# Kernel optimization log

Measured on AMD Instinct MI355X. Metric: run time of the kernel, lower is better.

Reference implementation:

```python
import jax, jax.numpy as jnp
import numpy as np

DIM = 1024
HEADS = 16
DIM_HEAD = 64
INNER = HEADS * DIM_HEAD  # 1024
SCALE = 1.0 / DIM_HEAD ** 0.5


def setup_inputs() -> dict:
    key = jax.random.key(0)
    ks = jax.random.split(key, 5)
    x = jax.random.normal(ks[0], (4, 2048, DIM), dtype=jnp.float32)
    # nn.Linear weights stored as [out, in]; we keep [in, out] for x @ W
    Wq = jax.random.normal(ks[1], (DIM, INNER), dtype=jnp.float32) * (1.0 / np.sqrt(DIM))
    Wkv = jax.random.normal(ks[2], (DIM, 2 * INNER), dtype=jnp.float32) * (1.0 / np.sqrt(DIM))
    Wo = jax.random.normal(ks[3], (INNER, DIM), dtype=jnp.float32) * (1.0 / np.sqrt(INNER))
    bo = jax.random.normal(ks[4], (DIM,), dtype=jnp.float32) * 0.01
    return {"x": x, "Wq": Wq, "Wkv": Wkv, "Wo": Wo, "bo": bo}


def reference(x, Wq, Wkv, Wo, bo):
    b, n, _ = x.shape
    q = x @ Wq                      # [b, n, inner]
    kv = x @ Wkv                    # [b, n, 2*inner]
    k, v = jnp.split(kv, 2, axis=2)
    # 'b n (h d) -> b h n d'
    q = q.reshape(b, n, HEADS, DIM_HEAD).transpose(0, 2, 1, 3)
    k = k.reshape(b, n, HEADS, DIM_HEAD).transpose(0, 2, 1, 3)
    v = v.reshape(b, n, HEADS, DIM_HEAD).transpose(0, 2, 1, 3)
    scores = jnp.einsum('bhid,bhjd->bhij', q, k) * SCALE  # [b,h,n,n]
    attn = jax.nn.softmax(scores, axis=-1)
    out = jnp.einsum('bhij,bhjd->bhid', attn, v)          # [b,h,n,d]
    out = out.transpose(0, 2, 1, 3).reshape(b, n, INNER)  # 'b h n d -> b n (h d)'
    return out @ Wo + bo
```

## Files before the change

kernel.cpp:

```cpp
#include <hip/hip_runtime.h>
#include <hip/hip_bf16.h>

typedef unsigned short u16;
typedef unsigned int u32;
typedef __attribute__((ext_vector_type(8))) short s8v;
typedef __attribute__((ext_vector_type(4))) float f4v;
typedef __attribute__((ext_vector_type(4))) unsigned short u16x4;

#define MFMA16(a,b,c) __builtin_amdgcn_mfma_f32_16x16x32_bf16((a),(b),(c),0,0,0)

#define TOKENS 8192
#define SEQ    2048
#define NH     16
#define DH     64
#define DIMK   1024
#define QPRE   0.18033688f

#if defined(__has_builtin)
#if __has_builtin(__builtin_amdgcn_exp2f)
#define EXP2(x) __builtin_amdgcn_exp2f(x)
#else
#define EXP2(x) __expf((x) * 0.69314718f)
#endif
#else
#define EXP2(x) __expf((x) * 0.69314718f)
#endif

__device__ __forceinline__ u16 f2bf(float x){
  union { float f; u32 u; } v; v.f = x;
  u32 r = v.u + 0x7FFFu + ((v.u >> 16) & 1u);
  return (u16)(r >> 16);
}

__device__ __forceinline__ void gld16(const u16* g, u16* s){
  __builtin_amdgcn_global_load_lds(
      (const __attribute__((address_space(1))) unsigned int*)(const void*)g,
      (__attribute__((address_space(3))) unsigned int*)(void*)s,
      16, 0, 0);
}

__global__ __launch_bounds__(256) void k_cast(const float* __restrict__ src,
                                              u16* __restrict__ dst){
  int i = (blockIdx.x * 256 + threadIdx.x) * 4;
  float4 v = *(const float4*)(src + i);
  u16x4 vh;
  float a[4] = {v.x, v.y, v.z, v.w};
#pragma unroll
  for (int j = 0; j < 4; j++) vh[j] = f2bf(a[j]);
  *(u16x4*)(dst + i) = vh;
}

__global__ __launch_bounds__(256) void k_transpose(const float* __restrict__ s0, int c0,
                                                   const float* __restrict__ s1, int c1,
                                                   int K, u16* __restrict__ dh){
  __shared__ float tile[64][65];
  int nb = blockIdx.x * 64, kb = blockIdx.y * 64;
  int tr = threadIdx.x >> 6, tc = threadIdx.x & 63;
#pragma unroll
  for (int i = 0; i < 16; i++){
    int k = kb + tr + i * 4, n = nb + tc;
    float v = (n < c0) ? s0[(size_t)k * c0 + n] : s1[(size_t)k * c1 + (n - c0)];
    tile[tr + i * 4][tc] = v;
  }
  __syncthreads();
#pragma unroll
  for (int i = 0; i < 16; i++){
    int nl = tr + i * 4, kl = tc;
    dh[(size_t)(nb + nl) * K + (kb + kl)] = f2bf(tile[kl][nl]);
  }
}

__global__ __launch_bounds__(256) void k_gemm(
    const u16* __restrict__ A, const u16* __restrict__ B, int nx,
    int mode, const float* __restrict__ bias, float* __restrict__ Cf,
    u16* __restrict__ Qh, u16* __restrict__ Kh, u16* __restrict__ Vth)
{
  __shared__ u16 sA[2][128*32], sB[2][128*32];
  const int tid = threadIdx.x, wave = tid >> 6, lane = tid & 63;
  const int lm = lane & 15, quad = lane >> 4;

  const int bid = blockIdx.x;
  const int xcd = bid & 7, slot = bid >> 3;
  const int gpx = nx >> 3;
  const int xt = xcd * gpx + slot % gpx;
  const int yt = slot / gpx;
  const int m0 = yt * 128, n0 = xt * 128;

  const int cof = (lane & 3) * 8;
  const int rsub = lane >> 2;

  f4v acc[4][4];
#pragma unroll
  for (int i = 0; i < 4; i++)
#pragma unroll
    for (int j = 0; j < 4; j++) acc[i][j] = (f4v){0.f, 0.f, 0.f, 0.f};

  const int wm = (wave >> 1) * 64, wn = (wave & 1) * 64;

  for (int kc = 0; kc < 16; kc++){
    int k = kc * 64;
#pragma unroll
    for (int cc = 0; cc < 2; cc++)
#pragma unroll
      for (int half = 0; half < 2; half++){
        int rb = wave * 32 + half * 16;
        int r = rb + rsub;
        gld16(A + (size_t)(m0 + r) * DIMK + k + cc * 32 + cof, &sA[cc][rb * 32]);
        gld16(B + (size_t)(n0 + r) * DIMK + k + cc * 32 + cof, &sB[cc][rb * 32]);
      }
    __syncthreads();

#pragma unroll
    for (int cc = 0; cc < 2; cc++){
      s8v ah[4], bh[4];
#pragma unroll
      for (int i = 0; i < 4; i++){
        ah[i] = *(const s8v*)&sA[cc][(wm + i * 16 + lm) * 32 + quad * 8];
        bh[i] = *(const s8v*)&sB[cc][(wn + i * 16 + lm) * 32 + quad * 8];
      }
#pragma unroll
      for (int i = 0; i < 4; i++)
#pragma unroll
        for (int j = 0; j < 4; j++)
          acc[i][j] = MFMA16(ah[i], bh[j], acc[i][j]);
    }
    __syncthreads();
  }

  if (mode == 1){
#pragma unroll
    for (int i = 0; i < 4; i++)
#pragma unroll
      for (int j = 0; j < 4; j++){
        int gn = n0 + wn + j * 16 + lm;
        float bv = bias[gn];
#pragma unroll
        for (int r = 0; r < 4; r++){
          int gm = m0 + wm + i * 16 + quad * 4 + r;
          Cf[(size_t)gm * DIMK + gn] = acc[i][j][r] + bv;
        }
      }
  } else {
#pragma unroll
    for (int i = 0; i < 4; i++)
#pragma unroll
      for (int j = 0; j < 4; j++){
        int gn = n0 + wn + j * 16 + lm;
#pragma unroll
        for (int r = 0; r < 4; r++){
          int gm = m0 + wm + i * 16 + quad * 4 + r;
          float v = acc[i][j][r];
          if (gn < 1024){
            Qh[(size_t)gm * DIMK + gn] = f2bf(v * QPRE);
          } else if (gn < 2048){
            Kh[(size_t)gm * DIMK + (gn - 1024)] = f2bf(v);
          } else {
            int df = gn - 2048;
            int hh = df >> 6, dd = df & 63;
            int bb = gm >> 11, ii = gm & 2047;
            int ip = (ii & ~31) | (((ii & 15) << 1) | ((ii >> 4) & 1));
            Vth[(size_t)((bb * NH + hh) * DH + dd) * SEQ + ip] = f2bf(v);
          }
        }
      }
  }
}

__global__ __launch_bounds__(256, 4) void k_attn(
    const u16* __restrict__ Qh, const u16* __restrict__ Kh, const u16* __restrict__ Vth,
    u16* __restrict__ Oh)
{
  __shared__ u16 sK[2*64*32];
  __shared__ u16 sV[2*64*32];
  __shared__ u16 sP[2*128*32];
  u32* sPd = (u32*)sP;

  const int bid = blockIdx.x;
  const int xcd = bid & 7, slot = bid >> 3;
  const int g = xcd * 8 + (slot >> 4);
  const int qt = slot & 15;
  const int b = g >> 4, h = g & 15;

  const int tid = threadIdx.x, wave = tid >> 6, lane = tid & 63;
  const int lm = lane & 15, quad = lane >> 4;
  const int tok0 = b * SEQ + qt * 128;
  const int cof = (lane & 3) * 8;
  const int rsub = lane >> 2;

  s8v qf[2][2];
#pragma unroll
  for (int c = 0; c < 2; c++)
#pragma unroll
    for (int ifr = 0; ifr < 2; ifr++){
      size_t ga = (size_t)(tok0 + wave * 32 + ifr * 16 + lm) * DIMK + h * DH + c * 32 + quad * 8;
      qf[c][ifr] = *(const s8v*)(Qh + ga);
    }

  const f4v fz = (f4v){0.f, 0.f, 0.f, 0.f};

  float lpart[2][4];
  f4v oacc[2][4];
#pragma unroll
  for (int ifr = 0; ifr < 2; ifr++){
#pragma unroll
    for (int r = 0; r < 4; r++) lpart[ifr][r] = 0.f;
#pragma unroll
    for (int fd = 0; fd < 4; fd++) oacc[ifr][fd] = (f4v){0.f, 0.f, 0.f, 0.f};
  }

  for (int kt = 0; kt < 32; kt++){
    int j0 = kt * 64;
#pragma unroll
    for (int c = 0; c < 2; c++){
      size_t gk = (size_t)(b * SEQ + j0 + wave * 16 + rsub) * DIMK + h * DH + c * 32 + cof;
      gld16(Kh + gk, &sK[c * 2048 + wave * 512]);
      size_t gv = (size_t)((b * NH + h) * DH + wave * 16 + rsub) * SEQ + j0 + c * 32 + cof;
      gld16(Vth + gv, &sV[c * 2048 + wave * 512]);
    }
    __syncthreads();

    f4v s[2][4];
#pragma unroll
    for (int fn = 0; fn < 4; fn++){
      s8v kh0 = *(const s8v*)&sK[0 * 2048 + (fn * 16 + lm) * 32 + quad * 8];
      s8v kh1 = *(const s8v*)&sK[1 * 2048 + (fn * 16 + lm) * 32 + quad * 8];
#pragma unroll
      for (int ifr = 0; ifr < 2; ifr++){
        s[ifr][fn] = MFMA16(qf[0][ifr], kh0, fz);
        s[ifr][fn] = MFMA16(qf[1][ifr], kh1, s[ifr][fn]);
      }
    }

#pragma unroll
    for (int ifr = 0; ifr < 2; ifr++){
#pragma unroll
      for (int fn = 0; fn < 4; fn++)
#pragma unroll
        for (int r = 0; r < 4; r++)
          s[ifr][fn][r] = EXP2(s[ifr][fn][r]);
      int rowb = wave * 32 + ifr * 16 + quad * 4;
#pragma unroll
      for (int r = 0; r < 4; r++)
#pragma unroll
        for (int jc = 0; jc < 2; jc++){
          union { float f; u32 u; } a0, a1;
          a0.f = s[ifr][jc * 2 + 0][r];
          a1.f = s[ifr][jc * 2 + 1][r];
          lpart[ifr][r] += a0.f + a1.f;
          sPd[jc * 2048 + (rowb + r) * 16 + lm] = __builtin_amdgcn_perm(a1.u, a0.u, 0x07060302);
        }
    }

#pragma unroll
    for (int c = 0; c < 2; c++)
#pragma unroll
      for (int ifr = 0; ifr < 2; ifr++){
        s8v ph = *(const s8v*)&sP[c * 4096 + (wave * 32 + ifr * 16 + lm) * 32 + quad * 8];
#pragma unroll
        for (int fd = 0; fd < 4; fd++){
          s8v vh = *(const s8v*)&sV[c * 2048 + (fd * 16 + lm) * 32 + quad * 8];
          oacc[ifr][fd] = MFMA16(ph, vh, oacc[ifr][fd]);
        }
      }
    __syncthreads();
  }

#pragma unroll
  for (int ifr = 0; ifr < 2; ifr++){
#pragma unroll
    for (int off = 1; off < 16; off <<= 1)
#pragma unroll
      for (int r = 0; r < 4; r++)
        lpart[ifr][r] += __shfl_xor(lpart[ifr][r], off, 64);
    float inv[4];
#pragma unroll
    for (int r = 0; r < 4; r++) inv[r] = 1.f / lpart[ifr][r];
#pragma unroll
    for (int fd = 0; fd < 4; fd++){
      int dcol = h * DH + fd * 16 + lm;
#pragma unroll
      for (int r = 0; r < 4; r++){
        int tok = tok0 + wave * 32 + ifr * 16 + quad * 4 + r;
        Oh[(size_t)tok * DIMK + dcol] = f2bf(oacc[ifr][fd][r] * inv[r]);
      }
    }
  }
}

extern "C" void kernel_launch(void* const* d_in, const int* in_sizes, int n_in,
                              void* d_out, int out_size, void* d_ws, size_t ws_size,
                              hipStream_t stream) {
  const float* x   = (const float*)d_in[0];
  const float* Wq  = (const float*)d_in[1];
  const float* Wkv = (const float*)d_in[2];
  const float* Wo  = (const float*)d_in[3];
  const float* bo  = (const float*)d_in[4];
  float* out = (float*)d_out;

  char* ws = (char*)d_ws;
  size_t off = 0;
  auto alloc = [&](size_t bytes) -> u16* {
    u16* p = (u16*)(ws + off);
    off += (bytes + 255) & ~(size_t)255;
    return p;
  };
  const size_t TK2 = (size_t)TOKENS * DIMK * 2;
  u16* xh  = alloc(TK2);
  u16* Wh  = alloc((size_t)3072 * DIMK * 2);
  u16* WOh = alloc((size_t)1024 * DIMK * 2);
  u16* Qh  = alloc(TK2);
  u16* Kh  = alloc(TK2);
  u16* Vth = alloc(TK2);
  u16* Oh  = alloc(TK2);

  k_cast<<<dim3((TOKENS * DIMK) / 1024), 256, 0, stream>>>(x, xh);
  k_transpose<<<dim3(48, 16), 256, 0, stream>>>(Wq, 1024, Wkv, 2048, DIMK, Wh);
  k_transpose<<<dim3(16, 16), 256, 0, stream>>>(Wo, 1024, Wo, 1024, DIMK, WOh);
  k_gemm<<<dim3(24 * 64), 256, 0, stream>>>(xh, Wh, 24, 0, nullptr, nullptr, Qh, Kh, Vth);
  k_attn<<<dim3(16 * NH * 4), 256, 0, stream>>>(Qh, Kh, Vth, Oh);
  k_gemm<<<dim3(8 * 64), 256, 0, stream>>>(Oh, WOh, 8, 1, bo, out, nullptr, nullptr, nullptr);
}
```

Baseline: 309.2 us.

## Double-buffer GEMM A tiles and attention K/V tiles, load B from global

```diff
diff --git a/kernel.cpp b/kernel.cpp
--- a/kernel.cpp
+++ b/kernel.cpp
@@ -71,19 +71,26 @@
 }
 
 __global__ __launch_bounds__(256) void k_gemm(
-    const u16* __restrict__ A, const u16* __restrict__ B, int nx,
+    const u16* __restrict__ A, const u16* __restrict__ B, int nx, int mpart,
     int mode, const float* __restrict__ bias, float* __restrict__ Cf,
     u16* __restrict__ Qh, u16* __restrict__ Kh, u16* __restrict__ Vth)
 {
-  __shared__ u16 sA[2][128*32], sB[2][128*32];
+  __shared__ u16 sA[2][2][128*32];
   const int tid = threadIdx.x, wave = tid >> 6, lane = tid & 63;
   const int lm = lane & 15, quad = lane >> 4;
 
   const int bid = blockIdx.x;
   const int xcd = bid & 7, slot = bid >> 3;
-  const int gpx = nx >> 3;
-  const int xt = xcd * gpx + slot % gpx;
-  const int yt = slot / gpx;
+  int xt, yt;
+  if (mpart == 0){
+    const int gpx = nx >> 3;
+    xt = xcd * gpx + slot % gpx;
+    yt = slot / gpx;
+  } else {
+    const int mg = (int)(gridDim.x >> 3) / nx;
+    xt = slot % nx;
+    yt = xcd * mg + slot / nx;
+  }
   const int m0 = yt * 128, n0 = xt * 128;
 
   const int cof = (lane & 3) * 8;
@@ -97,32 +104,44 @@
 
   const int wm = (wave >> 1) * 64, wn = (wave & 1) * 64;
 
-  for (int kc = 0; kc < 16; kc++){
+  auto stageA = [&](int kc, int db){
     int k = kc * 64;
 #pragma unroll
     for (int cc = 0; cc < 2; cc++)
 #pragma unroll
       for (int half = 0; half < 2; half++){
         int rb = wave * 32 + half * 16;
-        int r = rb + rsub;
-        gld16(A + (size_t)(m0 + r) * DIMK + k + cc * 32 + cof, &sA[cc][rb * 32]);
-        gld16(B + (size_t)(n0 + r) * DIMK + k + cc * 32 + cof, &sB[cc][rb * 32]);
-      }
-    __syncthreads();
+        gld16(A + (size_t)(m0 + rb + rsub) * DIMK + k + cc * 32 + cof,
+              &sA[db][cc][rb * 32]);
+      }
+  };
+
+  stageA(0, 0);
+  __syncthreads();
+
+  for (int kc = 0; kc < 16; kc++){
+    const int db = kc & 1;
+    if (kc + 1 < 16) stageA(kc + 1, db ^ 1);
+
+    s8v bfr[2][4];
+#pragma unroll
+    for (int cc = 0; cc < 2; cc++)
+#pragma unroll
+      for (int j = 0; j < 4; j++)
+        bfr[cc][j] = *(const s8v*)(B + (size_t)(n0 + wn + j * 16 + lm) * DIMK
+                                     + kc * 64 + cc * 32 + quad * 8);
 
 #pragma unroll
     for (int cc = 0; cc < 2; cc++){
-      s8v ah[4], bh[4];
-#pragma unroll
-      for (int i = 0; i < 4; i++){
-        ah[i] = *(const s8v*)&sA[cc][(wm + i * 16 + lm) * 32 + quad * 8];
-        bh[i] = *(const s8v*)&sB[cc][(wn + i * 16 + lm) * 32 + quad * 8];
-      }
+      s8v ah[4];
 #pragma unroll
       for (int i = 0; i < 4; i++)
+        ah[i] = *(const s8v*)&sA[db][cc][(wm + i * 16 + lm) * 32 + quad * 8];
+#pragma unroll
+      for (int i = 0; i < 4; i++)
 #pragma unroll
         for (int j = 0; j < 4; j++)
-          acc[i][j] = MFMA16(ah[i], bh[j], acc[i][j]);
+          acc[i][j] = MFMA16(ah[i], bfr[cc][j], acc[i][j]);
     }
     __syncthreads();
   }
@@ -166,12 +185,12 @@
   }
 }
 
-__global__ __launch_bounds__(256, 4) void k_attn(
+__global__ __launch_bounds__(256, 3) void k_attn(
     const u16* __restrict__ Qh, const u16* __restrict__ Kh, const u16* __restrict__ Vth,
     u16* __restrict__ Oh)
 {
-  __shared__ u16 sK[2*64*32];
-  __shared__ u16 sV[2*64*32];
+  __shared__ u16 sK[2][2*64*32];
+  __shared__ u16 sV[2][2*64*32];
   __shared__ u16 sP[2*128*32];
   u32* sPd = (u32*)sP;
 
@@ -208,22 +227,29 @@
     for (int fd = 0; fd < 4; fd++) oacc[ifr][fd] = (f4v){0.f, 0.f, 0.f, 0.f};
   }
 
-  for (int kt = 0; kt < 32; kt++){
+  auto stageKV = [&](int kt, int db){
     int j0 = kt * 64;
 #pragma unroll
     for (int c = 0; c < 2; c++){
       size_t gk = (size_t)(b * SEQ + j0 + wave * 16 + rsub) * DIMK + h * DH + c * 32 + cof;
-      gld16(Kh + gk, &sK[c * 2048 + wave * 512]);
+      gld16(Kh + gk, &sK[db][c * 2048 + wave * 512]);
       size_t gv = (size_t)((b * NH + h) * DH + wave * 16 + rsub) * SEQ + j0 + c * 32 + cof;
-      gld16(Vth + gv, &sV[c * 2048 + wave * 512]);
-    }
-    __syncthreads();
+      gld16(Vth + gv, &sV[db][c * 2048 + wave * 512]);
+    }
+  };
+
+  stageKV(0, 0);
+  __syncthreads();
+
+  for (int kt = 0; kt < 32; kt++){
+    const int db = kt & 1;
+    if (kt + 1 < 32) stageKV(kt + 1, db ^ 1);
 
     f4v s[2][4];
 #pragma unroll
     for (int fn = 0; fn < 4; fn++){
-      s8v kh0 = *(const s8v*)&sK[0 * 2048 + (fn * 16 + lm) * 32 + quad * 8];
-      s8v kh1 = *(const s8v*)&sK[1 * 2048 + (fn * 16 + lm) * 32 + quad * 8];
+      s8v kh0 = *(const s8v*)&sK[db][0 * 2048 + (fn * 16 + lm) * 32 + quad * 8];
+      s8v kh1 = *(const s8v*)&sK[db][1 * 2048 + (fn * 16 + lm) * 32 + quad * 8];
 #pragma unroll
       for (int ifr = 0; ifr < 2; ifr++){
         s[ifr][fn] = MFMA16(qf[0][ifr], kh0, fz);
@@ -258,7 +284,7 @@
         s8v ph = *(const s8v*)&sP[c * 4096 + (wave * 32 + ifr * 16 + lm) * 32 + quad * 8];
 #pragma unroll
         for (int fd = 0; fd < 4; fd++){
-          s8v vh = *(const s8v*)&sV[c * 2048 + (fd * 16 + lm) * 32 + quad * 8];
+          s8v vh = *(const s8v*)&sV[db][c * 2048 + (fd * 16 + lm) * 32 + quad * 8];
           oacc[ifr][fd] = MFMA16(ph, vh, oacc[ifr][fd]);
         }
       }
@@ -316,7 +342,9 @@
   k_cast<<<dim3((TOKENS * DIMK) / 1024), 256, 0, stream>>>(x, xh);
   k_transpose<<<dim3(48, 16), 256, 0, stream>>>(Wq, 1024, Wkv, 2048, DIMK, Wh);
   k_transpose<<<dim3(16, 16), 256, 0, stream>>>(Wo, 1024, Wo, 1024, DIMK, WOh);
-  k_gemm<<<dim3(24 * 64), 256, 0, stream>>>(xh, Wh, 24, 0, nullptr, nullptr, Qh, Kh, Vth);
+  k_gemm<<<dim3(24 * 64), 256, 0, stream>>>(xh, Wh, 24, 0, 0, nullptr, nullptr,
+                                            Qh, Kh, Vth);
   k_attn<<<dim3(16 * NH * 4), 256, 0, stream>>>(Qh, Kh, Vth, Oh);
-  k_gemm<<<dim3(8 * 64), 256, 0, stream>>>(Oh, WOh, 8, 1, bo, out, nullptr, nullptr, nullptr);
-}
+  k_gemm<<<dim3(8 * 64), 256, 0, stream>>>(Oh, WOh, 8, 1, 1, bo, out,
+                                           nullptr, nullptr, nullptr);
+}
```

Measured after the change: 373.4 us. 1.21x slower.
